# Performance work log

Measured on AMD Instinct MI355X. Metric: run time of the kernel, lower is better.

Reference implementation:

```python
import jax, jax.numpy as jnp
import numpy as np

B, N, F, D = 8, 2048, 128, 128


def setup_inputs() -> dict:
    key = jax.random.key(0)
    k1, k2, k3 = jax.random.split(key, 3)
    inputs = jax.random.normal(k1, (B, N, F), dtype=jnp.float32)
    adj = jax.random.uniform(k2, (B, N, N), dtype=jnp.float32)  # nonneg weights -> positive degrees
    W_kernel = jax.random.normal(k3, (F, D), dtype=jnp.float32) * (1.0 / np.sqrt(F))
    W_bias = jnp.zeros((D,), dtype=jnp.float32)
    return {"inputs": inputs, "adj": adj, "W_kernel": W_kernel, "W_bias": W_bias}


def _normalize_adjacency(adj):
    # D^{-1/2} A D^{-1/2}: same math as diag-matmul chain, via broadcast scaling
    d = jnp.sum(adj, axis=-1)                      # [B, N]
    d_sqrt_inv = jnp.power(d, -0.5)
    d_sqrt_inv = jnp.where(jnp.isinf(d_sqrt_inv), 0.0, d_sqrt_inv)
    return d_sqrt_inv[..., :, None] * adj * d_sqrt_inv[..., None, :]


def reference(inputs, adj, W_kernel, W_bias):
    adj_norm = _normalize_adjacency(adj)           # [B, N, N]
    feats = inputs @ W_kernel + W_bias             # [B, N, D]
    out = jnp.einsum('bnm,bmd->bnd', adj_norm, feats)
    return jax.nn.relu(out)
```

## Files before the change

### kernel.cpp

```cpp
#include <hip/hip_runtime.h>
#include <hip/hip_bf16.h>
#include <stdint.h>

#define B_ 8
#define N_ 2048
#define F_ 128
#define D_ 128

typedef short bf16x8 __attribute__((ext_vector_type(8)));
typedef float f32x4 __attribute__((ext_vector_type(4)));

__device__ __forceinline__ unsigned short f2bf(float f) {
    unsigned u = __float_as_uint(f);
    u += 0x7fffu + ((u >> 16) & 1u);
    return (unsigned short)(u >> 16);
}

__global__ __launch_bounds__(256) void k_degfeat(const float* __restrict__ adj,
                                                 const float* __restrict__ x,
                                                 const float* __restrict__ W,
                                                 const float* __restrict__ bias,
                                                 float* __restrict__ rs,
                                                 unsigned short* __restrict__ gt) {
    __shared__ __align__(16) unsigned char sX[64 * 128 * 2];
    __shared__ __align__(16) unsigned char sW[128 * 128 * 2];

    const int t = threadIdx.x;
    if (blockIdx.x < 4096) {
        const int wave = t >> 6, lane = t & 63;
        const int row = blockIdx.x * 4 + wave;
        const float4* p = (const float4*)(adj + (size_t)row * N_);
        float s = 0.f;
#pragma unroll
        for (int j = 0; j < 8; ++j) {
            float4 v = p[j * 64 + lane];
            s += (v.x + v.y) + (v.z + v.w);
        }
#pragma unroll
        for (int m = 1; m < 64; m <<= 1) s += __shfl_xor(s, m, 64);
        if (lane == 0) rs[row] = (s > 0.f) ? (1.0f / sqrtf(s)) : 0.f;
        return;
    }

    const int R0 = (blockIdx.x - 4096) * 64;

#pragma unroll
    for (int i = 0; i < 16; ++i) {
        int c = i * 256 + t;
        int f = c >> 5, d0 = (c & 31) * 4;
        float4 v = *(const float4*)(W + (size_t)f * D_ + d0);
        float vv[4] = {v.x, v.y, v.z, v.w};
#pragma unroll
        for (int e = 0; e < 4; ++e) {
            int dd = d0 + e;
            unsigned byte = (unsigned)(dd * 256 + f * 2);
            byte ^= ((byte >> 8) & 15u) << 4;
            *(unsigned short*)(sW + byte) = f2bf(vv[e]);
        }
    }
#pragma unroll
    for (int j = 0; j < 4; ++j) {
        int c = j * 256 + t;
        int row = c >> 4, sub = c & 15;
        const float4* src = (const float4*)(x + (size_t)(R0 + row) * F_ + sub * 8);
        float4 v0 = src[0], v1 = src[1];
        union { bf16x8 v; unsigned short u[8]; } pk;
        pk.u[0] = f2bf(v0.x); pk.u[1] = f2bf(v0.y); pk.u[2] = f2bf(v0.z); pk.u[3] = f2bf(v0.w);
        pk.u[4] = f2bf(v1.x); pk.u[5] = f2bf(v1.y); pk.u[6] = f2bf(v1.z); pk.u[7] = f2bf(v1.w);
        unsigned byte = (unsigned)(row * 256 + sub * 16);
        byte ^= ((byte >> 8) & 7u) << 4;
        *(bf16x8*)(sX + byte) = pk.v;
    }
    __syncthreads();

    const int w = t >> 6, l = t & 63, lr = l & 15, lh = l >> 4;
    f32x4 acc[8];
#pragma unroll
    for (int j = 0; j < 8; ++j) acc[j] = (f32x4){0.f, 0.f, 0.f, 0.f};

#pragma unroll
    for (int ks = 0; ks < 4; ++ks) {
        unsigned abyte = (unsigned)((w * 16 + lr) * 256 + lh * 16 + ks * 64);
        abyte ^= ((abyte >> 8) & 7u) << 4;
        bf16x8 a = *(const bf16x8*)(sX + abyte);
#pragma unroll
        for (int j = 0; j < 8; ++j) {
            unsigned bbyte = (unsigned)((j * 16 + lr) * 256 + lh * 16 + ks * 64);
            bbyte ^= ((bbyte >> 8) & 15u) << 4;
            bf16x8 bb = *(const bf16x8*)(sW + bbyte);
            acc[j] = __builtin_amdgcn_mfma_f32_16x16x32_bf16(a, bb, acc[j], 0, 0, 0);
        }
    }

#pragma unroll
    for (int j = 0; j < 8; ++j) {
        int d = j * 16 + lr;
        float bv = bias[d];
#pragma unroll
        for (int r = 0; r < 4; ++r) {
            int m = R0 + w * 16 + lh * 4 + r;
            int b = m >> 11, n = m & (N_ - 1);
            gt[((size_t)b * D_ + d) * N_ + n] = f2bf(acc[j][r] + bv);
        }
    }
}

__global__ __launch_bounds__(512, 1) void k_gcn(const float* __restrict__ adj,
                                                const unsigned short* __restrict__ gt,
                                                const float* __restrict__ rs,
                                                float* __restrict__ out) {
    __shared__ __align__(16) unsigned char sA[2][64 * 128 * 4];
    __shared__ __align__(16) unsigned char sB[2][128 * 128 * 2];
    __shared__ __align__(16) unsigned char sRS[N_ * 4];

    unsigned bid = blockIdx.x;
    unsigned wg = (bid & 7u) * 32u + (bid >> 3);
    const int b = (int)(wg >> 5);
    const int R0 = (int)(wg & 31u) * 64;

    const float* adjB = adj + (size_t)b * N_ * N_ + (size_t)R0 * N_;
    const unsigned short* gtB = gt + (size_t)b * D_ * N_;
    const float* rsB = rs + (size_t)b * N_;

    const int t = threadIdx.x;
    const int w = t >> 6, l = t & 63, lr = l & 15, lh = l >> 4;
    const int wr = w >> 2, wc = w & 3;

    auto stage = [&](int buf, int it) {
        const int k0 = it * 128;
        unsigned char* pA = sA[buf];
        unsigned char* pB = sB[buf];
#pragma unroll
        for (int i = 0; i < 4; ++i) {
            unsigned L = (unsigned)(i * 512 + t) * 16u;
            unsigned row = L >> 9, wi = L & 511u;
            unsigned wis = wi ^ ((row & 15u) << 4);
            const unsigned char* g = (const unsigned char*)adjB + (size_t)row * 8192 + (size_t)k0 * 4 + wis;
            __builtin_amdgcn_global_load_lds(
                (const __attribute__((address_space(1))) void*)g,
                (__attribute__((address_space(3))) void*)(pA + L), 16, 0, 0);
        }
#pragma unroll
        for (int i = 0; i < 4; ++i) {
            unsigned L = (unsigned)(i * 512 + t) * 16u;
            unsigned d = L >> 8, wi = L & 255u;
            unsigned wis = wi ^ ((d & 15u) << 4);
            const unsigned char* g = (const unsigned char*)gtB + (size_t)d * 4096 + (size_t)k0 * 2 + wis;
            __builtin_amdgcn_global_load_lds(
                (const __attribute__((address_space(1))) void*)g,
                (__attribute__((address_space(3))) void*)(pB + L), 16, 0, 0);
        }
    };

    {
        unsigned L = (unsigned)t * 16u;
        __builtin_amdgcn_global_load_lds(
            (const __attribute__((address_space(1))) void*)((const unsigned char*)rsB + L),
            (__attribute__((address_space(3))) void*)(sRS + L), 16, 0, 0);
    }
    stage(0, 0);
    stage(1, 1);

    f32x4 acc[2][2];
#pragma unroll
    for (int i = 0; i < 2; ++i)
#pragma unroll
        for (int jn = 0; jn < 2; ++jn) acc[i][jn] = (f32x4){0.f, 0.f, 0.f, 0.f};

    const int NITER = N_ / 128;
#pragma unroll
    for (int it = 0; it < NITER; ++it) {
        if (it == NITER - 1) {
            asm volatile("s_waitcnt vmcnt(0)" ::: "memory");
        } else {
            asm volatile("s_waitcnt vmcnt(8)" ::: "memory");
        }
        __builtin_amdgcn_s_barrier();
        asm volatile("" ::: "memory");
        __builtin_amdgcn_sched_barrier(0);

        const unsigned char* pA = sA[it & 1];
        const unsigned char* pB = sB[it & 1];
#pragma unroll
        for (int kk = 0; kk < 4; ++kk) {
            f32x4 r0 = *(const f32x4*)(sRS + it * 512 + kk * 128 + lh * 32);
            f32x4 r1 = *(const f32x4*)(sRS + it * 512 + kk * 128 + lh * 32 + 16);
            bf16x8 av[2];
#pragma unroll
            for (int i = 0; i < 2; ++i) {
                unsigned row = (unsigned)(wr * 32 + i * 16 + lr);
                unsigned base = row * 512 + (unsigned)(kk * 128 + lh * 32);
                unsigned swz = (row & 15u) << 4;
                f32x4 x0 = *(const f32x4*)(pA + (base ^ swz));
                f32x4 x1 = *(const f32x4*)(pA + ((base + 16) ^ swz));
                x0 *= r0; x1 *= r1;
                unsigned u0, u1, u2, u3;
                asm("v_cvt_pk_bf16_f32 %0, %1, %2" : "=v"(u0) : "v"(x0[0]), "v"(x0[1]));
                asm("v_cvt_pk_bf16_f32 %0, %1, %2" : "=v"(u1) : "v"(x0[2]), "v"(x0[3]));
                asm("v_cvt_pk_bf16_f32 %0, %1, %2" : "=v"(u2) : "v"(x1[0]), "v"(x1[1]));
                asm("v_cvt_pk_bf16_f32 %0, %1, %2" : "=v"(u3) : "v"(x1[2]), "v"(x1[3]));
                union { unsigned u[4]; bf16x8 v; } pk;
                pk.u[0] = u0; pk.u[1] = u1; pk.u[2] = u2; pk.u[3] = u3;
                av[i] = pk.v;
            }
            bf16x8 bv[2];
#pragma unroll
            for (int jn = 0; jn < 2; ++jn) {
                unsigned d = (unsigned)(wc * 32 + jn * 16 + lr);
                unsigned byte = d * 256 + (unsigned)(kk * 64 + lh * 16);
                byte ^= (d & 15u) << 4;
                bv[jn] = *(const bf16x8*)(pB + byte);
            }
#pragma unroll
            for (int i = 0; i < 2; ++i)
#pragma unroll
                for (int jn = 0; jn < 2; ++jn)
                    acc[i][jn] = __builtin_amdgcn_mfma_f32_16x16x32_bf16(av[i], bv[jn], acc[i][jn], 0, 0, 0);
        }

        asm volatile("s_waitcnt lgkmcnt(0)" ::: "memory");
        __builtin_amdgcn_sched_barrier(0);
        __builtin_amdgcn_s_barrier();
        if (it < NITER - 2) stage(it & 1, it + 2);
    }

#pragma unroll
    for (int i = 0; i < 2; ++i) {
#pragma unroll
        for (int reg = 0; reg < 4; ++reg) {
            int rowl = wr * 32 + i * 16 + lh * 4 + reg;
            float rsn = ((const float*)sRS)[R0 + rowl];
#pragma unroll
            for (int jn = 0; jn < 2; ++jn) {
                int d = wc * 32 + jn * 16 + lr;
                float v = acc[i][jn][reg] * rsn;
                out[((size_t)(b * N_ + R0 + rowl)) * D_ + d] = fmaxf(v, 0.f);
            }
        }
    }
}

extern "C" void kernel_launch(void* const* d_in, const int* in_sizes, int n_in,
                              void* d_out, int out_size, void* d_ws, size_t ws_size,
                              hipStream_t stream) {
    const float* inputs = (const float*)d_in[0];
    const float* adj    = (const float*)d_in[1];
    const float* Wk     = (const float*)d_in[2];
    const float* Wb     = (const float*)d_in[3];
    float* out = (float*)d_out;

    float* rs = (float*)d_ws;
    unsigned short* gt = (unsigned short*)((char*)d_ws + 65536);

    k_degfeat<<<4096 + 256, 256, 0, stream>>>(adj, inputs, Wk, Wb, rs, gt);
    k_gcn    <<<256, 512, 0, stream>>>(adj, gt, rs, out);
}
```

Measured before the change: 63.34 us.

## Stage adjacency through registers as bf16 into LDS, shrink LDS, reorder degfeat blocks

The GCN kernel now loads adjacency tiles into registers one iteration ahead, scales them by the column degree factor, converts to bf16 once, and writes them to LDS. Previously fp32 went directly to LDS and every wave rescaled and converted at MFMA time. This halves the A tile's LDS footprint and drops launch_bounds min-blocks 1, so more workgroups could be resident, but the software pipeline becomes one stage deep with register prefetch. It also moves the feature-GEMM blocks to the front of the degfeat grid so they start first.

```diff
diff --git a/kernel.cpp b/kernel.cpp
--- a/kernel.cpp
+++ b/kernel.cpp
@@ -26,9 +26,9 @@
     __shared__ __align__(16) unsigned char sW[128 * 128 * 2];
 
     const int t = threadIdx.x;
-    if (blockIdx.x < 4096) {
+    if (blockIdx.x >= 256) {
         const int wave = t >> 6, lane = t & 63;
-        const int row = blockIdx.x * 4 + wave;
+        const int row = (blockIdx.x - 256) * 4 + wave;
         const float4* p = (const float4*)(adj + (size_t)row * N_);
         float s = 0.f;
 #pragma unroll
@@ -42,7 +42,7 @@
         return;
     }
 
-    const int R0 = (blockIdx.x - 4096) * 64;
+    const int R0 = blockIdx.x * 64;
 
 #pragma unroll
     for (int i = 0; i < 16; ++i) {
@@ -105,13 +105,13 @@
     }
 }
 
-__global__ __launch_bounds__(512, 1) void k_gcn(const float* __restrict__ adj,
-                                                const unsigned short* __restrict__ gt,
-                                                const float* __restrict__ rs,
-                                                float* __restrict__ out) {
-    __shared__ __align__(16) unsigned char sA[2][64 * 128 * 4];
-    __shared__ __align__(16) unsigned char sB[2][128 * 128 * 2];
-    __shared__ __align__(16) unsigned char sRS[N_ * 4];
+__global__ __launch_bounds__(512) void k_gcn(const float* __restrict__ adj,
+                                             const unsigned short* __restrict__ gt,
+                                             const float* __restrict__ rs,
+                                             float* __restrict__ out) {
+    __shared__ __align__(16) unsigned char sA[2][64 * 256];
+    __shared__ __align__(16) unsigned char sB[2][128 * 256];
+    __shared__ __align__(16) float sRS[N_];
 
     unsigned bid = blockIdx.x;
     unsigned wg = (bid & 7u) * 32u + (bid >> 3);
@@ -126,40 +126,31 @@
     const int w = t >> 6, l = t & 63, lr = l & 15, lh = l >> 4;
     const int wr = w >> 2, wc = w & 3;
 
-    auto stage = [&](int buf, int it) {
-        const int k0 = it * 128;
-        unsigned char* pA = sA[buf];
+    const unsigned short* bSrc[4];
+    unsigned bL[4];
+#pragma unroll
+    for (int i = 0; i < 4; ++i) {
+        unsigned c = (unsigned)(i * 512 + t);
+        unsigned L = c * 16u;
+        unsigned lg = L ^ (((L >> 8) & 7u) << 4);
+        bL[i] = L;
+        bSrc[i] = gtB + (size_t)(lg >> 8) * N_ + ((lg & 255u) >> 1);
+    }
+    auto issueB = [&](int buf, int k0) {
         unsigned char* pB = sB[buf];
 #pragma unroll
         for (int i = 0; i < 4; ++i) {
-            unsigned L = (unsigned)(i * 512 + t) * 16u;
-            unsigned row = L >> 9, wi = L & 511u;
-            unsigned wis = wi ^ ((row & 15u) << 4);
-            const unsigned char* g = (const unsigned char*)adjB + (size_t)row * 8192 + (size_t)k0 * 4 + wis;
             __builtin_amdgcn_global_load_lds(
-                (const __attribute__((address_space(1))) void*)g,
-                (__attribute__((address_space(3))) void*)(pA + L), 16, 0, 0);
-        }
-#pragma unroll
-        for (int i = 0; i < 4; ++i) {
-            unsigned L = (unsigned)(i * 512 + t) * 16u;
-            unsigned d = L >> 8, wi = L & 255u;
-            unsigned wis = wi ^ ((d & 15u) << 4);
-            const unsigned char* g = (const unsigned char*)gtB + (size_t)d * 4096 + (size_t)k0 * 2 + wis;
-            __builtin_amdgcn_global_load_lds(
-                (const __attribute__((address_space(1))) void*)g,
-                (__attribute__((address_space(3))) void*)(pB + L), 16, 0, 0);
+                (const __attribute__((address_space(1))) void*)(bSrc[i] + k0),
+                (__attribute__((address_space(3))) void*)(pB + bL[i]), 16, 0, 0);
         }
     };
 
-    {
-        unsigned L = (unsigned)t * 16u;
-        __builtin_amdgcn_global_load_lds(
-            (const __attribute__((address_space(1))) void*)((const unsigned char*)rsB + L),
-            (__attribute__((address_space(3))) void*)(sRS + L), 16, 0, 0);
-    }
-    stage(0, 0);
-    stage(1, 1);
+    const float* aSrc = adjB + (size_t)(t >> 3) * N_ + (t & 7) * 16;
+    const unsigned aRow = (unsigned)(t >> 3);
+    const unsigned aBase = aRow * 256u + (unsigned)((t & 7) * 32);
+    const unsigned aSwz = (aRow & 7u) << 4;
+    const int rsIdx0 = (t & 7) * 4;
 
     f32x4 acc[2][2];
 #pragma unroll
@@ -167,73 +158,93 @@
 #pragma unroll
         for (int jn = 0; jn < 2; ++jn) acc[i][jn] = (f32x4){0.f, 0.f, 0.f, 0.f};
 
+    __builtin_amdgcn_global_load_lds(
+        (const __attribute__((address_space(1))) void*)((const unsigned char*)rsB + t * 16),
+        (__attribute__((address_space(3))) void*)((unsigned char*)sRS + t * 16), 16, 0, 0);
+    issueB(0, 0);
+    f32x4 aA[4];
+#pragma unroll
+    for (int j = 0; j < 4; ++j) aA[j] = *(const f32x4*)(aSrc + j * 4);
+    asm volatile("s_waitcnt vmcnt(8)" ::: "memory");
+    __builtin_amdgcn_s_barrier();
+
     const int NITER = N_ / 128;
-#pragma unroll
     for (int it = 0; it < NITER; ++it) {
-        if (it == NITER - 1) {
+        const int cur = it & 1;
+        f32x4 nA[4];
+#pragma unroll
+        for (int j = 0; j < 4; ++j) nA[j] = aA[j];
+        if (it + 1 < NITER) {
+            issueB(cur ^ 1, (it + 1) * 128);
+            const float* s = aSrc + (it + 1) * 128;
+#pragma unroll
+            for (int j = 0; j < 4; ++j) nA[j] = *(const f32x4*)(s + j * 4);
+            asm volatile("s_waitcnt vmcnt(8)" ::: "memory");
+        } else {
             asm volatile("s_waitcnt vmcnt(0)" ::: "memory");
-        } else {
-            asm volatile("s_waitcnt vmcnt(8)" ::: "memory");
-        }
+        }
+        __builtin_amdgcn_sched_barrier(0);
+
+        {
+            const f32x4* rsV = (const f32x4*)sRS + (it * 32 + rsIdx0);
+            unsigned u[8];
+#pragma unroll
+            for (int j = 0; j < 4; ++j) {
+                f32x4 xj = aA[j] * rsV[j];
+                asm("v_cvt_pk_bf16_f32 %0, %1, %2" : "=v"(u[2 * j]) : "v"(xj[0]), "v"(xj[1]));
+                asm("v_cvt_pk_bf16_f32 %0, %1, %2" : "=v"(u[2 * j + 1]) : "v"(xj[2]), "v"(xj[3]));
+            }
+            union { unsigned u[4]; bf16x8 v; } p0, p1;
+            p0.u[0] = u[0]; p0.u[1] = u[1]; p0.u[2] = u[2]; p0.u[3] = u[3];
+            p1.u[0] = u[4]; p1.u[1] = u[5]; p1.u[2] = u[6]; p1.u[3] = u[7];
+            *(bf16x8*)(sA[cur] + (aBase ^ aSwz)) = p0.v;
+            *(bf16x8*)(sA[cur] + ((aBase + 16) ^ aSwz)) = p1.v;
+        }
+        asm volatile("s_waitcnt lgkmcnt(0)" ::: "memory");
+        __builtin_amdgcn_sched_barrier(0);
         __builtin_amdgcn_s_barrier();
-        asm volatile("" ::: "memory");
-        __builtin_amdgcn_sched_barrier(0);
-
-        const unsigned char* pA = sA[it & 1];
-        const unsigned char* pB = sB[it & 1];
+
+        const unsigned char* pA = sA[cur];
+        const unsigned char* pB = sB[cur];
 #pragma unroll
         for (int kk = 0; kk < 4; ++kk) {
-            f32x4 r0 = *(const f32x4*)(sRS + it * 512 + kk * 128 + lh * 32);
-            f32x4 r1 = *(const f32x4*)(sRS + it * 512 + kk * 128 + lh * 32 + 16);
-            bf16x8 av[2];
+            bf16x8 a[2], bb[2];
 #pragma unroll
             for (int i = 0; i < 2; ++i) {
                 unsigned row = (unsigned)(wr * 32 + i * 16 + lr);
-                unsigned base = row * 512 + (unsigned)(kk * 128 + lh * 32);
-                unsigned swz = (row & 15u) << 4;
-                f32x4 x0 = *(const f32x4*)(pA + (base ^ swz));
-                f32x4 x1 = *(const f32x4*)(pA + ((base + 16) ^ swz));
-                x0 *= r0; x1 *= r1;
-                unsigned u0, u1, u2, u3;
-                asm("v_cvt_pk_bf16_f32 %0, %1, %2" : "=v"(u0) : "v"(x0[0]), "v"(x0[1]));
-                asm("v_cvt_pk_bf16_f32 %0, %1, %2" : "=v"(u1) : "v"(x0[2]), "v"(x0[3]));
-                asm("v_cvt_pk_bf16_f32 %0, %1, %2" : "=v"(u2) : "v"(x1[0]), "v"(x1[1]));
-                asm("v_cvt_pk_bf16_f32 %0, %1, %2" : "=v"(u3) : "v"(x1[2]), "v"(x1[3]));
-                union { unsigned u[4]; bf16x8 v; } pk;
-                pk.u[0] = u0; pk.u[1] = u1; pk.u[2] = u2; pk.u[3] = u3;
-                av[i] = pk.v;
-            }
-            bf16x8 bv[2];
+                unsigned byte = row * 256 + (unsigned)(kk * 64 + lh * 16);
+                byte ^= (row & 7u) << 4;
+                a[i] = *(const bf16x8*)(pA + byte);
+            }
 #pragma unroll
             for (int jn = 0; jn < 2; ++jn) {
                 unsigned d = (unsigned)(wc * 32 + jn * 16 + lr);
                 unsigned byte = d * 256 + (unsigned)(kk * 64 + lh * 16);
-                byte ^= (d & 15u) << 4;
-                bv[jn] = *(const bf16x8*)(pB + byte);
+                byte ^= (d & 7u) << 4;
+                bb[jn] = *(const bf16x8*)(pB + byte);
             }
 #pragma unroll
             for (int i = 0; i < 2; ++i)
 #pragma unroll
                 for (int jn = 0; jn < 2; ++jn)
-                    acc[i][jn] = __builtin_amdgcn_mfma_f32_16x16x32_bf16(av[i], bv[jn], acc[i][jn], 0, 0, 0);
-        }
-
-        asm volatile("s_waitcnt lgkmcnt(0)" ::: "memory");
-        __builtin_amdgcn_sched_barrier(0);
+                    acc[i][jn] = __builtin_amdgcn_mfma_f32_16x16x32_bf16(a[i], bb[jn], acc[i][jn], 0, 0, 0);
+        }
         __builtin_amdgcn_s_barrier();
-        if (it < NITER - 2) stage(it & 1, it + 2);
+
+#pragma unroll
+        for (int j = 0; j < 4; ++j) aA[j] = nA[j];
     }
 
 #pragma unroll
     for (int i = 0; i < 2; ++i) {
 #pragma unroll
-        for (int reg = 0; reg < 4; ++reg) {
-            int rowl = wr * 32 + i * 16 + lh * 4 + reg;
-            float rsn = ((const float*)sRS)[R0 + rowl];
+        for (int r = 0; r < 4; ++r) {
+            int rowl = wr * 32 + i * 16 + lh * 4 + r;
+            float rsn = sRS[R0 + rowl];
 #pragma unroll
             for (int jn = 0; jn < 2; ++jn) {
                 int d = wc * 32 + jn * 16 + lr;
-                float v = acc[i][jn][reg] * rsn;
+                float v = acc[i][jn][r] * rsn;
                 out[((size_t)(b * N_ + R0 + rowl)) * D_ + d] = fmaxf(v, 0.f);
             }
         }
@@ -252,6 +263,6 @@
     float* rs = (float*)d_ws;
     unsigned short* gt = (unsigned short*)((char*)d_ws + 65536);
 
-    k_degfeat<<<4096 + 256, 256, 0, stream>>>(adj, inputs, Wk, Wb, rs, gt);
+    k_degfeat<<<256 + 4096, 256, 0, stream>>>(adj, inputs, Wk, Wb, rs, gt);
     k_gcn    <<<256, 512, 0, stream>>>(adj, gt, rs, out);
 }
```

Result: faster. 62.09 us (-2.0%).
